# Kernel tuning notes

Hardware: AMD Instinct MI355X
Metric: run time of the kernel (lower is better)

## Reference

```python
import jax, jax.numpy as jnp
import numpy as np
from jax import lax

B, T, F, K = 128, 1024, 128, 32


def setup_inputs() -> dict:
    key = jax.random.key(0)
    k1, k2, k3 = jax.random.split(key, 3)
    inp = jax.random.normal(k1, (B, T, F), dtype=jnp.float32)
    mask = jnp.ones((B, T), dtype=bool)
    W_emit = jax.random.normal(k2, (F, K), dtype=jnp.float32) * 0.02
    transition = jax.random.normal(k3, (K, K), dtype=jnp.float32) * 0.1
    return {"input": inp, "mask": mask, "W_emit": W_emit, "transition": transition}


def reference(input, mask, W_emit, transition):
    # emissions: [B, T, K]
    emission = jnp.einsum('btf,fk->btk', input, W_emit)
    alpha0 = emission[:, 0]                      # [B, K]
    em_seq = jnp.swapaxes(emission[:, 1:], 0, 1)  # [T-1, B, K]
    mk_seq = jnp.swapaxes(mask[:, 1:], 0, 1)      # [T-1, B]

    def step(alpha, xs):
        em_t, m_t = xs
        # alpha_t[b,j] = logsumexp_i(alpha[b,i] + transition[i,j]) + em_t[b,j]
        new = jax.scipy.special.logsumexp(alpha[:, :, None] + transition[None], axis=1) + em_t
        alpha = jnp.where(m_t[:, None], new, alpha)
        return alpha, None

    alpha, _ = lax.scan(step, alpha0, (em_seq, mk_seq))
    log_z = jax.scipy.special.logsumexp(alpha, axis=-1)  # [B]
    return jnp.sum(log_z)
```

## Files before the change

kernel.cpp:

```cpp
#include <hip/hip_runtime.h>

#define Bb 128
#define Tt 1024
#define Ff 128
#define Kk 32
#define SXS 130
#define KS 36
#define KE 36
#define LOG32 3.4657359027997265f

typedef __attribute__((ext_vector_type(8))) short bf16x8;
typedef __attribute__((ext_vector_type(4))) float f32x4;

__device__ __forceinline__ float bf2f(unsigned u) {
    return __uint_as_float(u << 16);
}
__device__ __forceinline__ unsigned short f2bf(float f) {
    unsigned u = __float_as_uint(f);
    u = (u + 0x7fffu + ((u >> 16) & 1u)) >> 16;
    return (unsigned short)u;
}
__device__ __forceinline__ unsigned bfpk(float a, float b) {
    unsigned ua = (__float_as_uint(a) + 0x8000u) >> 16;
    unsigned ub = (__float_as_uint(b) + 0x8000u) & 0xffff0000u;
    return ua | ub;
}

__global__ __launch_bounds__(128) void emis_kernel(
    const float* __restrict__ inp, const float* __restrict__ W,
    unsigned short* __restrict__ em)
{
    __shared__ float xs[64 * SXS];
    __shared__ __align__(16) float Wl[Ff * Kk];
    const int tid = threadIdx.x;

    #pragma unroll
    for (int i = 0; i < 8; ++i) {
        int idx = (tid + i * 128) * 4;
        *(float4*)&Wl[idx] = *(const float4*)&W[idx];
    }
    const float* gx = inp + (long)blockIdx.x * 64 * Ff;
    #pragma unroll
    for (int i = 0; i < 16; ++i) {
        int id = tid + i * 128;
        float4 v = ((const float4*)gx)[id];
        int row = id >> 5;
        int col = (id & 31) * 4;
        float* dst = &xs[row * SXS + col];
        *(float2*)dst       = make_float2(v.x, v.y);
        *(float2*)(dst + 2) = make_float2(v.z, v.w);
    }
    __syncthreads();

    const int k4 = (tid & 7) * 4;
    const int rg = tid >> 3;
    const int r0 = rg * 4;
    const long grow0 = (long)blockIdx.x * 64 + r0;

    float acc[4][4];
    #pragma unroll
    for (int r = 0; r < 4; ++r)
        #pragma unroll
        for (int j = 0; j < 4; ++j) acc[r][j] = 0.f;

    #pragma unroll 2
    for (int f = 0; f < Ff; f += 4) {
        float4 w0 = *(const float4*)&Wl[(f + 0) * Kk + k4];
        float4 w1 = *(const float4*)&Wl[(f + 1) * Kk + k4];
        float4 w2 = *(const float4*)&Wl[(f + 2) * Kk + k4];
        float4 w3 = *(const float4*)&Wl[(f + 3) * Kk + k4];
        #pragma unroll
        for (int r = 0; r < 4; ++r) {
            const float* xr = &xs[(r0 + r) * SXS + f];
            float2 xa = *(const float2*)xr;
            float2 xb = *(const float2*)(xr + 2);
            acc[r][0] += xa.x * w0.x; acc[r][1] += xa.x * w0.y;
            acc[r][2] += xa.x * w0.z; acc[r][3] += xa.x * w0.w;
            acc[r][0] += xa.y * w1.x; acc[r][1] += xa.y * w1.y;
            acc[r][2] += xa.y * w1.z; acc[r][3] += xa.y * w1.w;
            acc[r][0] += xb.x * w2.x; acc[r][1] += xb.x * w2.y;
            acc[r][2] += xb.x * w2.z; acc[r][3] += xb.x * w2.w;
            acc[r][0] += xb.y * w3.x; acc[r][1] += xb.y * w3.y;
            acc[r][2] += xb.y * w3.z; acc[r][3] += xb.y * w3.w;
        }
    }
    #pragma unroll
    for (int r = 0; r < 4; ++r) {
        unsigned lo = bfpk(acc[r][0], acc[r][1]);
        unsigned hi = bfpk(acc[r][2], acc[r][3]);
        *(uint2*)&em[(grow0 + r) * Kk + k4] = make_uint2(lo, hi);
    }
}

__global__ __launch_bounds__(64) void chunk_kernel(
    const unsigned short* __restrict__ em, const int* __restrict__ mask,
    const float* __restrict__ trans, unsigned short* __restrict__ SQ)
{
    __shared__ __align__(16) float gl[32 * KE];
    __shared__ __align__(16) unsigned short Sl[32 * KS];
    const int lane = threadIdx.x & 63;
    const int q = lane >> 4, n = lane & 15;
    const int b = blockIdx.x >> 5, c = blockIdx.x & 31;
    const int t0 = c ? c * 32 : 1;
    const int L  = c ? 32 : 31;

    bf16x8 A0, A1;
    #pragma unroll
    for (int j = 0; j < 8; ++j) {
        A0[j] = (short)f2bf(__expf(trans[(q * 8 + j) * Kk + n]));
        A1[j] = (short)f2bf(__expf(trans[(q * 8 + j) * Kk + 16 + n]));
    }

    const unsigned short* emp = em + ((long)b * Tt + t0) * Kk;
    #pragma unroll
    for (int it = 0; it < 4; ++it) {
        int f = it * 256 + lane * 4;
        if (f < L * 32) {
            uint2 r = *(const uint2*)(emp + f);
            float4 v;
            v.x = __expf(bf2f(r.x & 0xffffu) - LOG32);
            v.y = __expf(bf2f(r.x >> 16)     - LOG32);
            v.z = __expf(bf2f(r.y & 0xffffu) - LOG32);
            v.w = __expf(bf2f(r.y >> 16)     - LOG32);
            *(float4*)&gl[(f >> 5) * KE + (f & 31)] = v;
        }
    }

    for (int i = lane; i < (32 * KS) / 2; i += 64)
        ((unsigned*)Sl)[i] = 0u;
    if (lane < 32) Sl[lane * KS + lane] = 0x3f80;

    const int* mbp = mask + (long)b * Tt;
    const f32x4 zz = {0.f, 0.f, 0.f, 0.f};

    for (int s = 0; s < L; ++s) {
        if (mbp[t0 + s] == 0) continue;
        uint2 xa = *(const uint2*)&Sl[ n       * KS + q * 8];
        uint2 xb = *(const uint2*)&Sl[ n       * KS + q * 8 + 4];
        uint2 ya = *(const uint2*)&Sl[(n + 16) * KS + q * 8];
        uint2 yb = *(const uint2*)&Sl[(n + 16) * KS + q * 8 + 4];
        uint4 u0 = make_uint4(xa.x, xa.y, xb.x, xb.y);
        uint4 u1 = make_uint4(ya.x, ya.y, yb.x, yb.y);
        bf16x8 B0 = __builtin_bit_cast(bf16x8, u0);
        bf16x8 B1 = __builtin_bit_cast(bf16x8, u1);
        f32x4 D00 = __builtin_amdgcn_mfma_f32_16x16x32_bf16(A0, B0, zz, 0, 0, 0);
        f32x4 D01 = __builtin_amdgcn_mfma_f32_16x16x32_bf16(A0, B1, zz, 0, 0, 0);
        f32x4 D10 = __builtin_amdgcn_mfma_f32_16x16x32_bf16(A1, B0, zz, 0, 0, 0);
        f32x4 D11 = __builtin_amdgcn_mfma_f32_16x16x32_bf16(A1, B1, zz, 0, 0, 0);
        float4 g0 = *(const float4*)&gl[s * KE + q * 4];
        float4 g1 = *(const float4*)&gl[s * KE + 16 + q * 4];
        *(uint2*)&Sl[ n       * KS      + q * 4] =
            make_uint2(bfpk(D00[0] * g0.x, D00[1] * g0.y), bfpk(D00[2] * g0.z, D00[3] * g0.w));
        *(uint2*)&Sl[(n + 16) * KS      + q * 4] =
            make_uint2(bfpk(D01[0] * g0.x, D01[1] * g0.y), bfpk(D01[2] * g0.z, D01[3] * g0.w));
        *(uint2*)&Sl[ n       * KS + 16 + q * 4] =
            make_uint2(bfpk(D10[0] * g1.x, D10[1] * g1.y), bfpk(D10[2] * g1.z, D10[3] * g1.w));
        *(uint2*)&Sl[(n + 16) * KS + 16 + q * 4] =
            make_uint2(bfpk(D11[0] * g1.x, D11[1] * g1.y), bfpk(D11[2] * g1.z, D11[3] * g1.w));
    }

    unsigned short* sq = SQ + (long)(b * 32 + c) * 1024;
    #pragma unroll
    for (int it = 0; it < 2; ++it) {
        int f = it * 512 + lane * 8;
        int kk = f >> 5, n0 = f & 31;
        unsigned v[4];
        #pragma unroll
        for (int e = 0; e < 4; ++e) {
            unsigned lo = Sl[(n0 + 2 * e    ) * KS + kk];
            unsigned hi = Sl[(n0 + 2 * e + 1) * KS + kk];
            v[e] = lo | (hi << 16);
        }
        *(uint4*)(sq + f) = make_uint4(v[0], v[1], v[2], v[3]);
    }
}

__global__ __launch_bounds__(64) void apply_kernel(
    const unsigned short* __restrict__ em, const int* __restrict__ mask,
    const unsigned short* __restrict__ SQ, float* __restrict__ out)
{
    const int b = blockIdx.x, lane = threadIdx.x & 63, k = lane & 31;
    const int* mbp = mask + (long)b * Tt;

    int cnt = 0;
    #pragma unroll
    for (int it = 0; it < 16; ++it) cnt += (mbp[it * 64 + lane] != 0) ? 1 : 0;
    #pragma unroll
    for (int off = 32; off; off >>= 1) cnt += __shfl_xor(cnt, off);
    cnt -= (mbp[0] != 0) ? 1 : 0;

    float a0 = bf2f(em[(long)b * Tt * Kk + k]);
    float c0 = __shfl(a0, 0);
    float p = __expf(a0 - c0);
    float csum = c0 + (float)cnt * LOG32;

    const unsigned short* sqb = SQ + (long)b * 32 * 1024;
    uint4 ra = *(const uint4*)(sqb + k * 32 +  0);
    uint4 rb = *(const uint4*)(sqb + k * 32 +  8);
    uint4 rc = *(const uint4*)(sqb + k * 32 + 16);
    uint4 rd = *(const uint4*)(sqb + k * 32 + 24);

    for (int c = 0; c < 32; ++c) {
        uint4 na, nb2, nc, nd;
        if (c + 1 < 32) {
            const unsigned short* s2 = sqb + (c + 1) * 1024 + k * 32;
            na  = *(const uint4*)(s2 +  0);
            nb2 = *(const uint4*)(s2 +  8);
            nc  = *(const uint4*)(s2 + 16);
            nd  = *(const uint4*)(s2 + 24);
        }
        const int pi = __float_as_int(p);
        float q0 = 0.f, q1 = 0.f, q2 = 0.f, q3 = 0.f;
        #define RL(j) __int_as_float(__builtin_amdgcn_readlane(pi, (j)))
        #define ACC2(word, j, acc) \
            acc = fmaf(bf2f((word) & 0xffffu), RL(j), acc); \
            acc = fmaf(bf2f((word) >> 16),     RL((j) + 1), acc);
        ACC2(ra.x,  0, q0) ACC2(ra.y,  2, q0) ACC2(ra.z,  4, q0) ACC2(ra.w,  6, q0)
        ACC2(rb.x,  8, q1) ACC2(rb.y, 10, q1) ACC2(rb.z, 12, q1) ACC2(rb.w, 14, q1)
        ACC2(rc.x, 16, q2) ACC2(rc.y, 18, q2) ACC2(rc.z, 20, q2) ACC2(rc.w, 22, q2)
        ACC2(rd.x, 24, q3) ACC2(rd.y, 26, q3) ACC2(rd.z, 28, q3) ACC2(rd.w, 30, q3)
        #undef ACC2
        #undef RL
        float qq = (q0 + q1) + (q2 + q3);
        float s0 = __int_as_float(__builtin_amdgcn_readlane(__float_as_int(qq), 0));
        csum += __logf(s0);
        p = qq * (1.0f / s0);
        ra = na; rb = nb2; rc = nc; rd = nd;
    }

    float sum = p;
    #pragma unroll
    for (int off = 16; off > 0; off >>= 1)
        sum += __shfl_xor(sum, off);
    if (lane == 0)
        atomicAdd(out, csum + __logf(sum));
}

extern "C" void kernel_launch(void* const* d_in, const int* in_sizes, int n_in,
                              void* d_out, int out_size, void* d_ws, size_t ws_size,
                              hipStream_t stream)
{
    const float* inp   = (const float*)d_in[0];
    const int*   mask  = (const int*)d_in[1];
    const float* W     = (const float*)d_in[2];
    const float* trans = (const float*)d_in[3];
    float* out = (float*)d_out;
    unsigned short* em = (unsigned short*)d_ws;
    unsigned short* SQ = (unsigned short*)((char*)d_ws + (size_t)Bb * Tt * Kk * 2);

    hipMemsetAsync(d_out, 0, sizeof(float), stream);
    emis_kernel<<<dim3(Bb * Tt / 64), dim3(128), 0, stream>>>(inp, W, em);
    chunk_kernel<<<dim3(Bb * 32), dim3(64), 0, stream>>>(em, mask, trans, SQ);
    apply_kernel<<<dim3(Bb), dim3(64), 0, stream>>>(em, mask, SQ, out);
}
```

Measured before the change: 151.6 us.

## Fuse emission GEMM into chunk kernel using bf16 MFMA, drop emis kernel

Removes the separate emission kernel and its bf16 intermediate buffer. Each chunk block now computes its 32x32 emission tile directly from the fp32 input with bf16 MFMA instructions, and apply_kernel computes the t=0 emission with a scalar dot product. This saves one launch and a global write/read round trip of the emission tensor. In exchange, W is re-read per block with strided scalar loads, and the input rows are read as uncoalesced per-lane float4 loads.

After: 133.9 us. -11.7%, faster.

```diff
diff --git a/kernel.cpp b/kernel.cpp
--- a/kernel.cpp
+++ b/kernel.cpp
@@ -4,7 +4,6 @@
 #define Tt 1024
 #define Ff 128
 #define Kk 32
-#define SXS 130
 #define KS 36
 #define KE 36
 #define LOG32 3.4657359027997265f
@@ -26,75 +25,10 @@
     return ua | ub;
 }
 
-__global__ __launch_bounds__(128) void emis_kernel(
-    const float* __restrict__ inp, const float* __restrict__ W,
-    unsigned short* __restrict__ em)
-{
-    __shared__ float xs[64 * SXS];
-    __shared__ __align__(16) float Wl[Ff * Kk];
-    const int tid = threadIdx.x;
-
-    #pragma unroll
-    for (int i = 0; i < 8; ++i) {
-        int idx = (tid + i * 128) * 4;
-        *(float4*)&Wl[idx] = *(const float4*)&W[idx];
-    }
-    const float* gx = inp + (long)blockIdx.x * 64 * Ff;
-    #pragma unroll
-    for (int i = 0; i < 16; ++i) {
-        int id = tid + i * 128;
-        float4 v = ((const float4*)gx)[id];
-        int row = id >> 5;
-        int col = (id & 31) * 4;
-        float* dst = &xs[row * SXS + col];
-        *(float2*)dst       = make_float2(v.x, v.y);
-        *(float2*)(dst + 2) = make_float2(v.z, v.w);
-    }
-    __syncthreads();
-
-    const int k4 = (tid & 7) * 4;
-    const int rg = tid >> 3;
-    const int r0 = rg * 4;
-    const long grow0 = (long)blockIdx.x * 64 + r0;
-
-    float acc[4][4];
-    #pragma unroll
-    for (int r = 0; r < 4; ++r)
-        #pragma unroll
-        for (int j = 0; j < 4; ++j) acc[r][j] = 0.f;
-
-    #pragma unroll 2
-    for (int f = 0; f < Ff; f += 4) {
-        float4 w0 = *(const float4*)&Wl[(f + 0) * Kk + k4];
-        float4 w1 = *(const float4*)&Wl[(f + 1) * Kk + k4];
-        float4 w2 = *(const float4*)&Wl[(f + 2) * Kk + k4];
-        float4 w3 = *(const float4*)&Wl[(f + 3) * Kk + k4];
-        #pragma unroll
-        for (int r = 0; r < 4; ++r) {
-            const float* xr = &xs[(r0 + r) * SXS + f];
-            float2 xa = *(const float2*)xr;
-            float2 xb = *(const float2*)(xr + 2);
-            acc[r][0] += xa.x * w0.x; acc[r][1] += xa.x * w0.y;
-            acc[r][2] += xa.x * w0.z; acc[r][3] += xa.x * w0.w;
-            acc[r][0] += xa.y * w1.x; acc[r][1] += xa.y * w1.y;
-            acc[r][2] += xa.y * w1.z; acc[r][3] += xa.y * w1.w;
-            acc[r][0] += xb.x * w2.x; acc[r][1] += xb.x * w2.y;
-            acc[r][2] += xb.x * w2.z; acc[r][3] += xb.x * w2.w;
-            acc[r][0] += xb.y * w3.x; acc[r][1] += xb.y * w3.y;
-            acc[r][2] += xb.y * w3.z; acc[r][3] += xb.y * w3.w;
-        }
-    }
-    #pragma unroll
-    for (int r = 0; r < 4; ++r) {
-        unsigned lo = bfpk(acc[r][0], acc[r][1]);
-        unsigned hi = bfpk(acc[r][2], acc[r][3]);
-        *(uint2*)&em[(grow0 + r) * Kk + k4] = make_uint2(lo, hi);
-    }
-}
-
-__global__ __launch_bounds__(64) void chunk_kernel(
-    const unsigned short* __restrict__ em, const int* __restrict__ mask,
-    const float* __restrict__ trans, unsigned short* __restrict__ SQ)
+__global__ __launch_bounds__(64, 4) void chunk_kernel(
+    const float* __restrict__ inp, const int* __restrict__ mask,
+    const float* __restrict__ W, const float* __restrict__ trans,
+    unsigned short* __restrict__ SQ)
 {
     __shared__ __align__(16) float gl[32 * KE];
     __shared__ __align__(16) unsigned short Sl[32 * KS];
@@ -111,19 +45,45 @@
         A1[j] = (short)f2bf(__expf(trans[(q * 8 + j) * Kk + 16 + n]));
     }
 
-    const unsigned short* emp = em + ((long)b * Tt + t0) * Kk;
-    #pragma unroll
-    for (int it = 0; it < 4; ++it) {
-        int f = it * 256 + lane * 4;
-        if (f < L * 32) {
-            uint2 r = *(const uint2*)(emp + f);
-            float4 v;
-            v.x = __expf(bf2f(r.x & 0xffffu) - LOG32);
-            v.y = __expf(bf2f(r.x >> 16)     - LOG32);
-            v.z = __expf(bf2f(r.y & 0xffffu) - LOG32);
-            v.w = __expf(bf2f(r.y >> 16)     - LOG32);
-            *(float4*)&gl[(f >> 5) * KE + (f & 31)] = v;
+    const f32x4 zz = {0.f, 0.f, 0.f, 0.f};
+    f32x4 E00 = zz, E01 = zz, E10 = zz, E11 = zz;
+    const float* xrow = inp + ((long)b * Tt + t0) * Ff;
+    #pragma unroll
+    for (int kt = 0; kt < 4; ++kt) {
+        const int f0 = kt * 32 + q * 8;
+        float4 al0 = *(const float4*)&xrow[ n        * Ff + f0];
+        float4 al1 = *(const float4*)&xrow[ n        * Ff + f0 + 4];
+        float4 ah0 = *(const float4*)&xrow[(n + 16)  * Ff + f0];
+        float4 ah1 = *(const float4*)&xrow[(n + 16)  * Ff + f0 + 4];
+        uint4 ua = make_uint4(bfpk(al0.x, al0.y), bfpk(al0.z, al0.w),
+                              bfpk(al1.x, al1.y), bfpk(al1.z, al1.w));
+        uint4 ub = make_uint4(bfpk(ah0.x, ah0.y), bfpk(ah0.z, ah0.w),
+                              bfpk(ah1.x, ah1.y), bfpk(ah1.z, ah1.w));
+        bf16x8 Alo = __builtin_bit_cast(bf16x8, ua);
+        bf16x8 Ahi = __builtin_bit_cast(bf16x8, ub);
+        float wl[8], wh[8];
+        #pragma unroll
+        for (int jj = 0; jj < 8; ++jj) {
+            wl[jj] = W[(f0 + jj) * Kk + n];
+            wh[jj] = W[(f0 + jj) * Kk + 16 + n];
         }
+        uint4 uc = make_uint4(bfpk(wl[0], wl[1]), bfpk(wl[2], wl[3]),
+                              bfpk(wl[4], wl[5]), bfpk(wl[6], wl[7]));
+        uint4 ud = make_uint4(bfpk(wh[0], wh[1]), bfpk(wh[2], wh[3]),
+                              bfpk(wh[4], wh[5]), bfpk(wh[6], wh[7]));
+        bf16x8 Blo = __builtin_bit_cast(bf16x8, uc);
+        bf16x8 Bhi = __builtin_bit_cast(bf16x8, ud);
+        E00 = __builtin_amdgcn_mfma_f32_16x16x32_bf16(Alo, Blo, E00, 0, 0, 0);
+        E01 = __builtin_amdgcn_mfma_f32_16x16x32_bf16(Alo, Bhi, E01, 0, 0, 0);
+        E10 = __builtin_amdgcn_mfma_f32_16x16x32_bf16(Ahi, Blo, E10, 0, 0, 0);
+        E11 = __builtin_amdgcn_mfma_f32_16x16x32_bf16(Ahi, Bhi, E11, 0, 0, 0);
+    }
+    #pragma unroll
+    for (int r = 0; r < 4; ++r) {
+        gl[( q * 4 + r)      * KE + n]      = __expf(E00[r] - LOG32);
+        gl[( q * 4 + r)      * KE + 16 + n] = __expf(E01[r] - LOG32);
+        gl[(16 + q * 4 + r)  * KE + n]      = __expf(E10[r] - LOG32);
+        gl[(16 + q * 4 + r)  * KE + 16 + n] = __expf(E11[r] - LOG32);
     }
 
     for (int i = lane; i < (32 * KS) / 2; i += 64)
@@ -131,7 +91,6 @@
     if (lane < 32) Sl[lane * KS + lane] = 0x3f80;
 
     const int* mbp = mask + (long)b * Tt;
-    const f32x4 zz = {0.f, 0.f, 0.f, 0.f};
 
     for (int s = 0; s < L; ++s) {
         if (mbp[t0 + s] == 0) continue;
@@ -176,29 +135,35 @@
 }
 
 __global__ __launch_bounds__(64) void apply_kernel(
-    const unsigned short* __restrict__ em, const int* __restrict__ mask,
-    const unsigned short* __restrict__ SQ, float* __restrict__ out)
+    const float* __restrict__ inp, const int* __restrict__ mask,
+    const float* __restrict__ W, const unsigned short* __restrict__ SQ,
+    float* __restrict__ out)
 {
     const int b = blockIdx.x, lane = threadIdx.x & 63, k = lane & 31;
     const int* mbp = mask + (long)b * Tt;
-
-    int cnt = 0;
-    #pragma unroll
-    for (int it = 0; it < 16; ++it) cnt += (mbp[it * 64 + lane] != 0) ? 1 : 0;
-    #pragma unroll
-    for (int off = 32; off; off >>= 1) cnt += __shfl_xor(cnt, off);
-    cnt -= (mbp[0] != 0) ? 1 : 0;
-
-    float a0 = bf2f(em[(long)b * Tt * Kk + k]);
-    float c0 = __shfl(a0, 0);
-    float p = __expf(a0 - c0);
-    float csum = c0 + (float)cnt * LOG32;
 
     const unsigned short* sqb = SQ + (long)b * 32 * 1024;
     uint4 ra = *(const uint4*)(sqb + k * 32 +  0);
     uint4 rb = *(const uint4*)(sqb + k * 32 +  8);
     uint4 rc = *(const uint4*)(sqb + k * 32 + 16);
     uint4 rd = *(const uint4*)(sqb + k * 32 + 24);
+
+    int cnt = 0;
+    #pragma unroll
+    for (int it = 0; it < 16; ++it) cnt += (mbp[it * 64 + lane] != 0) ? 1 : 0;
+    #pragma unroll
+    for (int off = 32; off; off >>= 1) cnt += __shfl_xor(cnt, off);
+    cnt -= (mbp[0] != 0) ? 1 : 0;
+
+    const float* x0 = inp + (long)b * Tt * Ff;
+    float a0 = 0.f;
+    #pragma unroll 4
+    for (int f = 0; f < Ff; ++f)
+        a0 = fmaf(x0[f], W[f * Kk + k], a0);
+
+    float c0 = __int_as_float(__builtin_amdgcn_readlane(__float_as_int(a0), 0));
+    float p = __expf(a0 - c0);
+    float csum = c0 + (float)cnt * LOG32;
 
     for (int c = 0; c < 32; ++c) {
         uint4 na, nb2, nc, nd;
@@ -245,11 +210,9 @@
     const float* W     = (const float*)d_in[2];
     const float* trans = (const float*)d_in[3];
     float* out = (float*)d_out;
-    unsigned short* em = (unsigned short*)d_ws;
-    unsigned short* SQ = (unsigned short*)((char*)d_ws + (size_t)Bb * Tt * Kk * 2);
+    unsigned short* SQ = (unsigned short*)d_ws;
 
     hipMemsetAsync(d_out, 0, sizeof(float), stream);
-    emis_kernel<<<dim3(Bb * Tt / 64), dim3(128), 0, stream>>>(inp, W, em);
-    chunk_kernel<<<dim3(Bb * 32), dim3(64), 0, stream>>>(em, mask, trans, SQ);
-    apply_kernel<<<dim3(Bb), dim3(64), 0, stream>>>(em, mask, SQ, out);
-}
+    chunk_kernel<<<dim3(Bb * 32), dim3(64), 0, stream>>>(inp, mask, W, trans, SQ);
+    apply_kernel<<<dim3(Bb), dim3(64), 0, stream>>>(inp, mask, W, SQ, out);
+}
```
